# Performance work log

Measured on AMD Instinct MI355X. Metric: run time of the kernel, lower is better.

Reference implementation:

```python
import jax, jax.numpy as jnp
import numpy as np

N, E, B = 16000, 256000, 64
H = 4
DIMS = [960, 512, 256, 128]  # per-layer input dims; output dim of layer i is DIMS[i+1] = HID[i]*H
HID = [128, 64, 32]


def setup_inputs() -> dict:
    key = jax.random.key(0)
    ks = jax.random.split(key, 16)
    inp = {}
    inp["x"] = jax.random.normal(ks[0], (N, DIMS[0]), jnp.float32)
    inp["edge_index"] = jax.random.randint(ks[1], (2, E), 0, N)
    inp["batch"] = jnp.sort(jax.random.randint(ks[2], (N,), 0, B))
    k = 3
    for i in range(3):
        din, c = DIMS[i], HID[i]
        s = 1.0 / np.sqrt(din).astype(np.float32)
        inp[f"Wl{i+1}"] = jax.random.normal(ks[k], (din, H * c), jnp.float32) * s; k += 1
        inp[f"Wr{i+1}"] = jax.random.normal(ks[k], (din, H * c), jnp.float32) * s; k += 1
        inp[f"att{i+1}"] = jax.random.normal(ks[k], (H, c), jnp.float32) * (1.0 / np.sqrt(c).astype(np.float32)); k += 1
        inp[f"b{i+1}"] = jnp.zeros((H * c,), jnp.float32)
        inp[f"gnw{i+1}"] = jnp.ones((H * c,), jnp.float32)
        inp[f"gnb{i+1}"] = jnp.zeros((H * c,), jnp.float32)
        inp[f"gnm{i+1}"] = jnp.ones((H * c,), jnp.float32)
    d = DIMS[-1]
    inp["aW1"] = jax.random.normal(ks[k], (d, 128), jnp.float32) * (1.0 / np.sqrt(d).astype(np.float32)); k += 1
    inp["ab1"] = jnp.zeros((128,), jnp.float32)
    inp["aW2"] = jax.random.normal(ks[k], (128, 1), jnp.float32) * (1.0 / np.sqrt(128).astype(np.float32)); k += 1
    inp["ab2"] = jnp.zeros((1,), jnp.float32)
    return inp


def _gatv2(x, src, dst, Wl, Wr, att, bias):
    # PyG GATv2Conv, concat=True, negative_slope=0.2 (self-loops already in src/dst)
    n = x.shape[0]
    h, c = att.shape
    xl = (x @ Wl).reshape(n, h, c)
    xr = (x @ Wr).reshape(n, h, c)
    e = jax.nn.leaky_relu(xl[src] + xr[dst], negative_slope=0.2)  # [E,H,C]
    logit = jnp.einsum('ehc,hc->eh', e, att)                      # [E,H]
    m = jax.ops.segment_max(logit, dst, num_segments=n)
    m = jnp.nan_to_num(m, neginf=0.0)
    p = jnp.exp(logit - m[dst])
    z = jax.ops.segment_sum(p, dst, num_segments=n)
    alpha = p / (z[dst] + 1e-16)                                  # segment softmax over dst
    out = jax.ops.segment_sum(alpha[:, :, None] * xl[src], dst, num_segments=n)
    return out.reshape(n, h * c) + bias


def _graphnorm(x, w, b, ms, eps=1e-5):
    # PyG GraphNorm with batch=None: normalize over all nodes as one graph
    mean = jnp.mean(x, axis=0, keepdims=True)
    xc = x - ms * mean
    var = jnp.mean(xc * xc, axis=0, keepdims=True)
    return w * xc / jnp.sqrt(var + eps) + b


def reference(x, edge_index, batch,
              Wl1, Wr1, att1, b1, gnw1, gnb1, gnm1,
              Wl2, Wr2, att2, b2, gnw2, gnb2, gnm2,
              Wl3, Wr3, att3, b3, gnw3, gnb3, gnm3,
              aW1, ab1, aW2, ab2):
    n = x.shape[0]
    loop = jnp.arange(n)
    src = jnp.concatenate([edge_index[0], loop])  # add self-loops (PyG default)
    dst = jnp.concatenate([edge_index[1], loop])
    layers = [(Wl1, Wr1, att1, b1, gnw1, gnb1, gnm1),
              (Wl2, Wr2, att2, b2, gnw2, gnb2, gnm2),
              (Wl3, Wr3, att3, b3, gnw3, gnb3, gnm3)]
    for Wl, Wr, att, bb, gw, gb, gm in layers:
        x = _gatv2(x, src, dst, Wl, Wr, att, bb)
        x = _graphnorm(x, gw, gb, gm)
        x = jax.nn.relu(x)
    # AttentionalAggregation pooling: gate MLP -> segment softmax over graphs -> weighted sum
    gate = jax.nn.relu(x @ aW1 + ab1) @ aW2 + ab2  # [N,1]
    mg = jax.ops.segment_max(gate, batch, num_segments=B)
    mg = jnp.nan_to_num(mg, neginf=0.0)
    pg = jnp.exp(gate - mg[batch])
    zg = jax.ops.segment_sum(pg, batch, num_segments=B)
    a = pg / (zg[batch] + 1e-16)
    return jax.ops.segment_sum(a * x, batch, num_segments=B)  # [B, 128]
```

## Files before the change

kernel.cpp:

```cpp
#include <hip/hip_runtime.h>
#include <cstdint>
#include <cstddef>
#include <math.h>


typedef _Float16  h16x8  __attribute__((ext_vector_type(8)));
typedef _Float16  h16x4  __attribute__((ext_vector_type(4)));
typedef _Float16  h16x2  __attribute__((ext_vector_type(2)));
typedef float     f32x4  __attribute__((ext_vector_type(4)));

template<int R> struct HV;
template<> struct HV<8> { using T = h16x8; };
template<> struct HV<4> { using T = h16x4; };
template<> struct HV<2> { using T = h16x2; };

__device__ __forceinline__ void gload_lds16(const void* g, void* l) {
    __builtin_amdgcn_global_load_lds(
        (const __attribute__((address_space(1))) uint32_t*)g,
        (__attribute__((address_space(3))) uint32_t*)l, 16, 0, 0);
}

__device__ __forceinline__ int swz_k(int k, int row) {
    return (k & ~31) | ((((k >> 3) & 3) ^ ((row >> 1) & 3)) << 3) | (k & 7);
}

__device__ __forceinline__ void gn_coef(float s1, float s2, float w, float b,
                                        float ms, float invN, float& al, float& be) {
    float mean = s1 * invN;
    float ex2  = s2 * invN;
    float a    = ms * mean;
    float var  = ex2 - 2.f * a * mean + a * a;
    al = w * rsqrtf(var + 1e-5f);
    be = b - a * al;
}

__device__ __forceinline__ void conv_elem(int t, const float* __restrict__ Wl,
                                          const float* __restrict__ Wr,
                                          _Float16* __restrict__ Wt, int K, int HC) {
    int k = t / HC, n = t - k * HC;
    const int ks = swz_k(k, n);
    Wt[(size_t)n * K + ks] = (_Float16)Wl[t];
    if (Wr) Wt[(size_t)(HC + n) * K + ks] = (_Float16)Wr[t];
}

__global__ __launch_bounds__(256) void conv_all(
        const float* __restrict__ Wl0, const float* __restrict__ Wr0, _Float16* __restrict__ T0,
        const float* __restrict__ Wl1, const float* __restrict__ Wr1, _Float16* __restrict__ T1,
        const float* __restrict__ Wl2, const float* __restrict__ Wr2, _Float16* __restrict__ T2,
        const float* __restrict__ Wa, _Float16* __restrict__ Ta) {
    int t = blockIdx.x * blockDim.x + threadIdx.x;
    if (t < 491520) { conv_elem(t, Wl0, Wr0, T0, 960, 512); return; }
    t -= 491520;
    if (t < 131072) { conv_elem(t, Wl1, Wr1, T1, 512, 256); return; }
    t -= 131072;
    if (t < 32768)  { conv_elem(t, Wl2, Wr2, T2, 256, 128); return; }
    t -= 32768;
    if (t < 16384)  conv_elem(t, Wa, nullptr, Ta, 128, 128);
}

template<bool NORM>
__global__ __launch_bounds__(256) void prep_a(
        const float* __restrict__ X,
        const float* __restrict__ s1, const float* __restrict__ s2,
        const float* __restrict__ gw, const float* __restrict__ gb,
        const float* __restrict__ gm, float invN,
        _Float16* __restrict__ Out, int M, int K) {
    int t = blockIdx.x * blockDim.x + threadIdx.x;
    const int gpr = K >> 3;
    if (t >= M * gpr) return;
    int m = t / gpr, g = t - m * gpr;
    int k = g << 3;
    const float* src = X + (size_t)m * K + k;
    float4 u0 = *(const float4*)src;
    float4 u1 = *(const float4*)(src + 4);
    float uu[8] = {u0.x, u0.y, u0.z, u0.w, u1.x, u1.y, u1.z, u1.w};
    if (NORM) {
        #pragma unroll
        for (int j = 0; j < 8; ++j) {
            float al, be;
            gn_coef(s1[k + j], s2[k + j], gw[k + j], gb[k + j], gm[k + j],
                    invN, al, be);
            uu[j] = fmaxf(al * uu[j] + be, 0.f);
        }
    }
    h16x8 h;
    #pragma unroll
    for (int j = 0; j < 8; ++j) h[j] = (_Float16)uu[j];
    *(h16x8*)&Out[(size_t)m * K + swz_k(k, m)] = h;
}

template<bool BIAS, bool RELU, bool GATE, typename OutT>
__global__ __launch_bounds__(256) void mfma_gemm(
        const _Float16* __restrict__ A, const _Float16* __restrict__ Bt,
        const float* __restrict__ bias, OutT* __restrict__ C,
        int M, int K, int N,
        const float* __restrict__ gw2, const float* __restrict__ gb2,
        float* __restrict__ gate) {
    __shared__ __attribute__((aligned(16))) _Float16 sA[2][128 * 32];
    __shared__ __attribute__((aligned(16))) _Float16 sB[2][128 * 32];
    __shared__ float gsum[128];

    const int gx  = gridDim.x;
    const int nwg = gx * gridDim.y;
    const int id  = blockIdx.y * gx + blockIdx.x;
    const int q   = nwg >> 3, r = nwg & 7;
    const int xcd = id & 7, sub = id >> 3;
    const int nid = (xcd < r) ? (xcd * (q + 1) + sub)
                              : (r * (q + 1) + (xcd - r) * q + sub);
    const int row0 = (nid / gx) * 128;
    const int col0 = (nid % gx) * 128;

    const int tid  = threadIdx.x;
    const int lane = tid & 63;
    const int w    = tid >> 6;
    const int wm   = w >> 1, wn = w & 1;
    const int lr   = lane & 15, lg = lane >> 4;
    const int bRow = w * 16 + (lane >> 2);
    const int bGrp = (lane & 3) * 8;
    const int fGrp = (lg ^ ((lr >> 1) & 3)) * 8;

    f32x4 acc[4][4] = {};

    const _Float16* pa = A  + (size_t)(row0 + bRow) * K + bGrp;
    const _Float16* pb = Bt + (size_t)(col0 + bRow) * K + bGrp;

    auto stage = [&](int buf, int k0) {
        gload_lds16(pa + k0,                  (char*)&sA[buf][0] + w * 1024);
        gload_lds16(pa + (size_t)64 * K + k0, (char*)&sA[buf][0] + 4096 + w * 1024);
        gload_lds16(pb + k0,                  (char*)&sB[buf][0] + w * 1024);
        gload_lds16(pb + (size_t)64 * K + k0, (char*)&sB[buf][0] + 4096 + w * 1024);
    };

    stage(0, 0);
    if (GATE) { if (tid < 128) gsum[tid] = 0.f; }
    __syncthreads();
    int cur = 0;
    for (int k0 = 0; k0 < K; k0 += 32) {
        if (k0 + 32 < K) stage(cur ^ 1, k0 + 32);
        h16x8 ah[4], bh[4];
        #pragma unroll
        for (int i = 0; i < 4; ++i) {
            ah[i] = *(const h16x8*)&sA[cur][(wm * 64 + i * 16 + lr) * 32 + fGrp];
            bh[i] = *(const h16x8*)&sB[cur][(wn * 64 + i * 16 + lr) * 32 + fGrp];
        }
        #pragma unroll
        for (int i = 0; i < 4; ++i)
            #pragma unroll
            for (int j = 0; j < 4; ++j)
                acc[i][j] = __builtin_amdgcn_mfma_f32_16x16x32_f16(ah[i], bh[j], acc[i][j], 0, 0, 0);
        __syncthreads();
        cur ^= 1;
    }

    if constexpr (!GATE) {
        #pragma unroll
        for (int i = 0; i < 4; ++i) {
            const int rowb = row0 + wm * 64 + i * 16 + lg * 4;
            #pragma unroll
            for (int j = 0; j < 4; ++j) {
                const int col = col0 + wn * 64 + j * 16 + lr;
                const float bv = BIAS ? bias[col] : 0.f;
                #pragma unroll
                for (int qq = 0; qq < 4; ++qq) {
                    float v = acc[i][j][qq] + bv;
                    if (RELU) v = fmaxf(v, 0.f);
                    C[(size_t)(rowb + qq) * N + col] = (OutT)v;
                }
            }
        }
    } else {
        float gp[4][4] = {};
        float w2[4];
        #pragma unroll
        for (int j = 0; j < 4; ++j) w2[j] = gw2[wn * 64 + j * 16 + lr];
        #pragma unroll
        for (int i = 0; i < 4; ++i)
            #pragma unroll
            for (int j = 0; j < 4; ++j) {
                const int col = wn * 64 + j * 16 + lr;
                const float bv = bias[col];
                #pragma unroll
                for (int qq = 0; qq < 4; ++qq) {
                    float v = fmaxf(acc[i][j][qq] + bv, 0.f);
                    gp[i][qq] += v * w2[j];
                }
            }
        #pragma unroll
        for (int i = 0; i < 4; ++i)
            #pragma unroll
            for (int qq = 0; qq < 4; ++qq) {
                float p = gp[i][qq];
                p += __shfl_xor(p, 1);
                p += __shfl_xor(p, 2);
                p += __shfl_xor(p, 4);
                p += __shfl_xor(p, 8);
                if (lr == 0) atomicAdd(&gsum[wm * 64 + i * 16 + lg * 4 + qq], p);
            }
        __syncthreads();
        if (tid < 128) gate[row0 + tid] = gsum[tid] + gb2[0];
    }
}

__global__ void csr_count(const int* __restrict__ edst, int E, int Etot,
                          int* __restrict__ deg) {
    int e = blockIdx.x * blockDim.x + threadIdx.x;
    if (e >= Etot) return;
    int d = (e < E) ? edst[e] : e - E;
    atomicAdd(&deg[d], 1);
}

__global__ __launch_bounds__(1024) void scan_deg(const int* __restrict__ deg,
                                                 int* __restrict__ row_start,
                                                 int* __restrict__ cursor, int N) {
    __shared__ int part[1024];
    const int tid = threadIdx.x;
    const int base = tid * 16;
    int loc[16];
    int s = 0;
    #pragma unroll
    for (int j = 0; j < 16; ++j) {
        int i = base + j;
        s += (i < N) ? deg[i] : 0;
        loc[j] = s;
    }
    part[tid] = s; __syncthreads();
    #pragma unroll
    for (int off = 1; off < 1024; off <<= 1) {
        int t2 = (tid >= off) ? part[tid - off] : 0;
        __syncthreads();
        part[tid] += t2;
        __syncthreads();
    }
    const int pre = tid ? part[tid - 1] : 0;
    #pragma unroll
    for (int j = 0; j < 16; ++j) {
        int i = base + j;
        if (i < N) {
            int st = pre + (j ? loc[j - 1] : 0);
            row_start[i] = st;
            cursor[i]    = st;
            if (i == N - 1) row_start[N] = pre + loc[j];
        }
    }
}

__global__ void csr_fill(const int* __restrict__ esrc, const int* __restrict__ edst,
                         int E, int Etot, int* __restrict__ cursor,
                         int* __restrict__ src_perm) {
    int e = blockIdx.x * blockDim.x + threadIdx.x;
    if (e >= Etot) return;
    int s, d;
    if (e < E) { s = esrc[e]; d = edst[e]; }
    else       { s = d = e - E; }
    int pos = atomicAdd(&cursor[d], 1);
    src_perm[pos] = s;
}

template<int LOG2C>
__global__ __launch_bounds__(256) void gat_agg(
        const _Float16* __restrict__ xlr,
        const float* __restrict__ att, const float* __restrict__ bias,
        const int* __restrict__ row_start, const int* __restrict__ src_perm,
        int N, float* __restrict__ out) {
    constexpr int HC  = 4 << LOG2C;
    constexpr int R   = HC / 64;
    constexpr int P   = R / 2;
    constexpr int STR = 2 * HC;
    constexpr int U   = 8;
    using hvec = typename HV<R>::T;

    const int widx = threadIdx.x >> 6;
    const int lane = threadIdx.x & 63;
    const int dst  = blockIdx.x * 4 + widx;
    if (dst >= N) return;

    const int base = lane * R;
    h16x2 xr2[P], at2[P];
    float acc[R];
    {
        hvec xv = *(const hvec*)&xlr[(size_t)dst * STR + HC + base];
        const h16x2* xp = (const h16x2*)&xv;
        #pragma unroll
        for (int i = 0; i < P; ++i) {
            xr2[i] = xp[i];
            h16x2 t;
            t[0] = (_Float16)att[base + 2 * i];
            t[1] = (_Float16)att[base + 2 * i + 1];
            at2[i] = t;
        }
        #pragma unroll
        for (int it = 0; it < R; ++it) acc[it] = 0.f;
    }
    h16x2 zp; zp[0] = (_Float16)0.f;  zp[1] = (_Float16)0.f;
    h16x2 sl; sl[0] = (_Float16)0.2f; sl[1] = (_Float16)0.2f;

    float z = 0.f;
    const int start = row_start[dst], end = row_start[dst + 1];

    auto do_edge = [&](const hvec& row) {
        const h16x2* r2 = (const h16x2*)&row;
        float a = 0.f;
        #pragma unroll
        for (int i = 0; i < P; ++i) {
            h16x2 s  = r2[i] + xr2[i];
            h16x2 lk = __builtin_elementwise_max(s, zp)
                     + __builtin_elementwise_min(s, zp) * sl;
            a = __builtin_amdgcn_fdot2(lk, at2[i], a, false);
        }
        #pragma unroll
        for (int sh = 1; sh < 16; sh <<= 1) a += __shfl_xor(a, sh);
        float p = __expf(a);
        z += p;
        #pragma unroll
        for (int it = 0; it < R; ++it) acc[it] += p * (float)row[it];
    };

    int cs = start;
    for (; cs + U <= end; cs += U) {
        hvec rows[U];
        #pragma unroll
        for (int k = 0; k < U; ++k) {
            int src = __builtin_amdgcn_readfirstlane(src_perm[cs + k]);
            rows[k] = *(const hvec*)&xlr[(size_t)src * STR + base];
        }
        #pragma unroll
        for (int k = 0; k < U; ++k) do_edge(rows[k]);
    }
    for (; cs < end; ++cs) {
        int src = __builtin_amdgcn_readfirstlane(src_perm[cs]);
        hvec row = *(const hvec*)&xlr[(size_t)src * STR + base];
        do_edge(row);
    }

    const float inv = 1.f / (z + 1e-16f);
    float ov[R];
    #pragma unroll
    for (int it = 0; it < R; ++it) ov[it] = acc[it] * inv + bias[base + it];
    float* po = out + (size_t)dst * HC + base;
    if constexpr (R == 8) {
        *(float4*)po       = make_float4(ov[0], ov[1], ov[2], ov[3]);
        *(float4*)(po + 4) = make_float4(ov[4], ov[5], ov[6], ov[7]);
    } else if constexpr (R == 4) {
        *(float4*)po = make_float4(ov[0], ov[1], ov[2], ov[3]);
    } else {
        *(float2*)po = make_float2(ov[0], ov[1]);
    }
}

__global__ __launch_bounds__(64) void colstats(const float* __restrict__ x, int HC,
                                               float* __restrict__ s1, float* __restrict__ s2) {
    int c  = blockIdx.x * 64 + threadIdx.x;
    int r0 = blockIdx.y * 128;
    float a = 0.f, b = 0.f;
    for (int r = r0; r < r0 + 128; ++r) {
        float v = x[(size_t)r * HC + c];
        a += v; b += v * v;
    }
    atomicAdd(&s1[c], a);
    atomicAdd(&s2[c], b);
}

__global__ __launch_bounds__(1024) void attn_pool(
        const float* __restrict__ x,
        const float* __restrict__ s1, const float* __restrict__ s2,
        const float* __restrict__ gw, const float* __restrict__ gb,
        const float* __restrict__ gm, float invN,
        const float* __restrict__ gate, const int* __restrict__ batch,
        int N, float* __restrict__ out) {
    const int b   = blockIdx.x;
    const int tid = threadIdx.x;
    const int grp = tid >> 7;
    const int ch  = tid & 127;
    int lo, hi;
    { int l = 0, r = N; while (l < r) { int mid = (l + r) >> 1; if (batch[mid] < b) l = mid + 1; else r = mid; } lo = l; }
    { int l = lo, r = N; while (l < r) { int mid = (l + r) >> 1; if (batch[mid] < b + 1) l = mid + 1; else r = mid; } hi = l; }
    if (lo >= hi) { if (tid < 128) out[b * 128 + tid] = 0.f; return; }

    float alc, bec;
    gn_coef(s1[ch], s2[ch], gw[ch], gb[ch], gm[ch], invN, alc, bec);

    __shared__ float red[1024];
    float mx = -INFINITY;
    for (int n = lo + tid; n < hi; n += 1024) mx = fmaxf(mx, gate[n]);
    red[tid] = mx; __syncthreads();
    for (int s = 512; s; s >>= 1) { if (tid < s) red[tid] = fmaxf(red[tid], red[tid + s]); __syncthreads(); }
    mx = red[0]; __syncthreads();
    float zs = 0.f;
    for (int n = lo + tid; n < hi; n += 1024) zs += __expf(gate[n] - mx);
    red[tid] = zs; __syncthreads();
    for (int s = 512; s; s >>= 1) { if (tid < s) red[tid] += red[tid + s]; __syncthreads(); }
    zs = red[0]; __syncthreads();
    float acc = 0.f;
    for (int n = lo + grp; n < hi; n += 8) {
        float wv = __expf(gate[n] - mx);
        float v  = fmaxf(alc * x[(size_t)n * 128 + ch] + bec, 0.f);
        acc += wv * v;
    }
    red[tid] = acc; __syncthreads();
    if (tid < 128) {
        float s = red[tid];
        #pragma unroll
        for (int g = 1; g < 8; ++g) s += red[g * 128 + tid];
        out[b * 128 + tid] = s / (zs + 1e-16f);
    }
}

extern "C" void kernel_launch(void* const* d_in, const int* in_sizes, int n_in,
                              void* d_out, int out_size, void* d_ws, size_t ws_size,
                              hipStream_t stream) {
    const float* x0  = (const float*)d_in[0];
    const int* edge  = (const int*)d_in[1];
    const int* batch = (const int*)d_in[2];
    const int N = in_sizes[2];
    const int E = in_sizes[1] / 2;
    const int Etot = E + N;
    const int dims[4] = {960, 512, 256, 128};

    const float* Wl[3]   = {(const float*)d_in[3],  (const float*)d_in[10], (const float*)d_in[17]};
    const float* Wr[3]   = {(const float*)d_in[4],  (const float*)d_in[11], (const float*)d_in[18]};
    const float* attp[3] = {(const float*)d_in[5],  (const float*)d_in[12], (const float*)d_in[19]};
    const float* bi[3]   = {(const float*)d_in[6],  (const float*)d_in[13], (const float*)d_in[20]};
    const float* gw[3]   = {(const float*)d_in[7],  (const float*)d_in[14], (const float*)d_in[21]};
    const float* gb[3]   = {(const float*)d_in[8],  (const float*)d_in[15], (const float*)d_in[22]};
    const float* gm[3]   = {(const float*)d_in[9],  (const float*)d_in[16], (const float*)d_in[23]};
    const float* aW1 = (const float*)d_in[24];
    const float* ab1 = (const float*)d_in[25];
    const float* aW2 = (const float*)d_in[26];
    const float* ab2 = (const float*)d_in[27];

    size_t off = 0;
    auto alloc = [&](size_t bytes) -> char* {
        char* p = (char*)d_ws + off;
        off += (bytes + 255) & ~(size_t)255;
        return p;
    };
    _Float16* xlr     = (_Float16*)alloc((size_t)N * 1024 * 2);
    _Float16* aT      = (_Float16*)alloc((size_t)N * 960 * 2);
    float*   bufC     = (float*)alloc((size_t)N * 512 * 4);
    int*     deg      = (int*)alloc((size_t)N * 4);
    int*     row_start= (int*)alloc((size_t)(N + 1) * 4);
    int*     cursor   = (int*)alloc((size_t)N * 4);
    int*     src_perm = (int*)alloc((size_t)Etot * 4);
    float*   s12      = (float*)alloc(3 * 1024 * 4);
    float*   gateB    = (float*)alloc((size_t)N * 4);
    _Float16* wt[3];
    for (int l = 0; l < 3; ++l)
        wt[l] = (_Float16*)alloc((size_t)dims[l] * (2 * dims[l + 1]) * 2);
    _Float16* awt = (_Float16*)alloc(128 * 128 * 2);
    (void)ws_size; (void)n_in; (void)out_size;

    const float invN = 1.0f / N;

    conv_all<<<(671744 + 255) / 256, 256, 0, stream>>>(
        Wl[0], Wr[0], wt[0], Wl[1], Wr[1], wt[1], Wl[2], Wr[2], wt[2], aW1, awt);

    hipMemsetAsync(deg, 0, (size_t)N * sizeof(int), stream);
    hipMemsetAsync(s12, 0, 3 * 1024 * sizeof(float), stream);
    csr_count<<<(Etot + 255) / 256, 256, 0, stream>>>(edge + E, E, Etot, deg);
    scan_deg<<<1, 1024, 0, stream>>>(deg, row_start, cursor, N);
    csr_fill<<<(Etot + 255) / 256, 256, 0, stream>>>(edge, edge + E, E, Etot,
                                                     cursor, src_perm);

    for (int l = 0; l < 3; ++l) {
        const int K = dims[l], HC = dims[l + 1];
        const int ngrp = N * (K >> 3);
        if (l == 0)
            prep_a<false><<<(ngrp + 255) / 256, 256, 0, stream>>>(
                x0, nullptr, nullptr, nullptr, nullptr, nullptr, 0.f, aT, N, K);
        else
            prep_a<true><<<(ngrp + 255) / 256, 256, 0, stream>>>(
                bufC, s12 + (l - 1) * 1024, s12 + (l - 1) * 1024 + 512,
                gw[l - 1], gb[l - 1], gm[l - 1], invN, aT, N, K);

        dim3 ggrid((2 * HC) / 128, N / 128);
        mfma_gemm<false, false, false, _Float16><<<ggrid, 256, 0, stream>>>(
            aT, wt[l], nullptr, xlr, N, K, 2 * HC, nullptr, nullptr, nullptr);

        const int agrid = (N + 3) / 4;
        if (l == 0)      gat_agg<7><<<agrid, 256, 0, stream>>>(xlr, attp[l], bi[l], row_start, src_perm, N, bufC);
        else if (l == 1) gat_agg<6><<<agrid, 256, 0, stream>>>(xlr, attp[l], bi[l], row_start, src_perm, N, bufC);
        else             gat_agg<5><<<agrid, 256, 0, stream>>>(xlr, attp[l], bi[l], row_start, src_perm, N, bufC);

        colstats<<<dim3(HC / 64, N / 128), 64, 0, stream>>>(bufC, HC, s12 + l * 1024, s12 + l * 1024 + 512);
    }

    prep_a<true><<<(N * 16 + 255) / 256, 256, 0, stream>>>(
        bufC, s12 + 2048, s12 + 2048 + 512, gw[2], gb[2], gm[2], invN, aT, N, 128);
    mfma_gemm<true, true, true, float><<<dim3(1, N / 128), 256, 0, stream>>>(
        aT, awt, ab1, nullptr, N, 128, 128, aW2, ab2, gateB);
    attn_pool<<<64, 1024, 0, stream>>>(bufC, s12 + 2048, s12 + 2048 + 512,
                                       gw[2], gb[2], gm[2], invN, gateB, batch, N, (float*)d_out);
}
```

Baseline: 326.9 us.

## Triple-buffer GEMM LDS staging with explicit vmcnt waits and raw barriers

Switches the MFMA GEMM from a double-buffered to a triple-buffered LDS pipeline that prefetches two K-tiles ahead. It waits with explicit s_waitcnt vmcnt counts and bare s_barrier in place of a full __syncthreads each iteration, so global loads can stay in flight across iterations. The cost is 50% more LDS per block, which may lower occupancy. Correctness also depends on each stage issuing exactly four loads, since the hand-written vmcnt values assume that count.

```diff
diff --git a/kernel.cpp b/kernel.cpp
--- a/kernel.cpp
+++ b/kernel.cpp
@@ -96,8 +96,8 @@
         int M, int K, int N,
         const float* __restrict__ gw2, const float* __restrict__ gb2,
         float* __restrict__ gate) {
-    __shared__ __attribute__((aligned(16))) _Float16 sA[2][128 * 32];
-    __shared__ __attribute__((aligned(16))) _Float16 sB[2][128 * 32];
+    __shared__ __attribute__((aligned(16))) _Float16 sA[3][128 * 32];
+    __shared__ __attribute__((aligned(16))) _Float16 sB[3][128 * 32];
     __shared__ float gsum[128];
 
     const int gx  = gridDim.x;
@@ -131,25 +131,44 @@
         gload_lds16(pb + (size_t)64 * K + k0, (char*)&sB[buf][0] + 4096 + w * 1024);
     };
 
+    const int n = K >> 5;
     stage(0, 0);
+    if (n > 1) stage(1, 32);
     if (GATE) { if (tid < 128) gsum[tid] = 0.f; }
-    __syncthreads();
-    int cur = 0;
-    for (int k0 = 0; k0 < K; k0 += 32) {
-        if (k0 + 32 < K) stage(cur ^ 1, k0 + 32);
+
+    int p = 0;
+    for (int i = 0; i < n; ++i) {
+        const int k0 = i << 5;
+        if (i + 2 < n) {
+            int pq = p + 2; if (pq >= 3) pq -= 3;
+            stage(pq, k0 + 64);
+            asm volatile("s_waitcnt vmcnt(8)" ::: "memory");
+        } else if (i + 1 < n) {
+            asm volatile("s_waitcnt vmcnt(4)" ::: "memory");
+        } else {
+            asm volatile("s_waitcnt vmcnt(0)" ::: "memory");
+        }
+        __builtin_amdgcn_sched_barrier(0);
+        __builtin_amdgcn_s_barrier();
+        __builtin_amdgcn_sched_barrier(0);
+
         h16x8 ah[4], bh[4];
         #pragma unroll
-        for (int i = 0; i < 4; ++i) {
-            ah[i] = *(const h16x8*)&sA[cur][(wm * 64 + i * 16 + lr) * 32 + fGrp];
-            bh[i] = *(const h16x8*)&sB[cur][(wn * 64 + i * 16 + lr) * 32 + fGrp];
-        }
-        #pragma unroll
-        for (int i = 0; i < 4; ++i)
+        for (int ii = 0; ii < 4; ++ii) {
+            ah[ii] = *(const h16x8*)&sA[p][(wm * 64 + ii * 16 + lr) * 32 + fGrp];
+            bh[ii] = *(const h16x8*)&sB[p][(wn * 64 + ii * 16 + lr) * 32 + fGrp];
+        }
+        #pragma unroll
+        for (int ii = 0; ii < 4; ++ii)
             #pragma unroll
-            for (int j = 0; j < 4; ++j)
-                acc[i][j] = __builtin_amdgcn_mfma_f32_16x16x32_f16(ah[i], bh[j], acc[i][j], 0, 0, 0);
-        __syncthreads();
-        cur ^= 1;
+            for (int jj = 0; jj < 4; ++jj)
+                acc[ii][jj] = __builtin_amdgcn_mfma_f32_16x16x32_f16(ah[ii], bh[jj], acc[ii][jj], 0, 0, 0);
+
+        asm volatile("s_waitcnt lgkmcnt(0)" ::: "memory");
+        __builtin_amdgcn_sched_barrier(0);
+        __builtin_amdgcn_s_barrier();
+        __builtin_amdgcn_sched_barrier(0);
+        ++p; if (p == 3) p = 0;
     }
 
     if constexpr (!GATE) {
@@ -189,12 +208,12 @@
         for (int i = 0; i < 4; ++i)
             #pragma unroll
             for (int qq = 0; qq < 4; ++qq) {
-                float p = gp[i][qq];
-                p += __shfl_xor(p, 1);
-                p += __shfl_xor(p, 2);
-                p += __shfl_xor(p, 4);
-                p += __shfl_xor(p, 8);
-                if (lr == 0) atomicAdd(&gsum[wm * 64 + i * 16 + lg * 4 + qq], p);
+                float pv = gp[i][qq];
+                pv += __shfl_xor(pv, 1);
+                pv += __shfl_xor(pv, 2);
+                pv += __shfl_xor(pv, 4);
+                pv += __shfl_xor(pv, 8);
+                if (lr == 0) atomicAdd(&gsum[wm * 64 + i * 16 + lg * 4 + qq], pv);
             }
         __syncthreads();
         if (tid < 128) gate[row0 + tid] = gsum[tid] + gb2[0];
```

After: 329.9 us. No clear change (+0.9%).
